# Optimization experiments

Hardware: AMD Instinct MI355X
Metric: run time of the kernel (lower is better)

Reference implementation:

```python
import jax, jax.numpy as jnp
import numpy as np

# The four fixed 2x2 patterns from the original module
PATTERNS = jnp.array([[[1, 2], [0, 0]],
                      [[0, 1], [0, 2]],
                      [[0, 0], [2, 1]],
                      [[2, 0], [1, 0]]], dtype=jnp.int32)


def setup_inputs() -> dict:
    key = jax.random.key(0)
    k1, k2 = jax.random.split(key)
    b, c, w, h = 32, 3, 1024, 1024
    x = jax.random.normal(k1, (b, c, w, h), dtype=jnp.float32)
    initmask = jax.random.randint(k2, (b, 1, w // 2, h // 2), 0, 4, dtype=jnp.int64)
    return {"x": x, "initmask": initmask}


def reference(x, initmask):
    b, c, w, h = x.shape
    # gather pattern per 2x2 block: (b, w/2, h/2, 2, 2)
    fm = PATTERNS[initmask[:, 0]]
    # interleave block dims back into full resolution: (b, 1, w, h)
    fm = fm.transpose(0, 1, 3, 2, 4).reshape(b, 1, w, h)
    mask1 = jnp.broadcast_to((fm == 1).astype(x.dtype), x.shape)
    mask2 = jnp.broadcast_to((fm == 2).astype(x.dtype), x.shape)
    return (mask1, mask2)
```

## Files before the change

kernel.cpp:

```cpp
#include <hip/hip_runtime.h>


#define N_F4_PER_OUT 25165824u

__global__ __launch_bounds__(256) void masksampling_kernel(const int* __restrict__ im,
                                                           float* __restrict__ out) {
    const unsigned t = blockIdx.x * 256u + threadIdx.x;
    const unsigned j  = t & 255u;
    const unsigned r  = (t >> 8) & 1023u;
    const unsigned bc = t >> 18;
    const unsigned b  = bc / 3u;

    const int2 m2 = ((const int2*)im)[b * 131072u + (r >> 1) * 256u + j];

    const unsigned base = (r & 1u) * 2u;
    const unsigned s0 = (unsigned)m2.x * 4u + base;
    const unsigned s1 = (unsigned)m2.y * 4u + base;

    const unsigned EQ1 = 0x4821u, EQ2 = 0x1482u;
    const float4 f1 = make_float4((float)((EQ1 >> s0) & 1u),
                                  (float)((EQ1 >> (s0 + 1u)) & 1u),
                                  (float)((EQ1 >> s1) & 1u),
                                  (float)((EQ1 >> (s1 + 1u)) & 1u));
    const float4 f2 = make_float4((float)((EQ2 >> s0) & 1u),
                                  (float)((EQ2 >> (s0 + 1u)) & 1u),
                                  (float)((EQ2 >> s1) & 1u),
                                  (float)((EQ2 >> (s1 + 1u)) & 1u));

    float4* o1 = (float4*)out;
    float4* o2 = o1 + N_F4_PER_OUT;
    o1[t] = f1;
    o2[t] = f2;
}

extern "C" void kernel_launch(void* const* d_in, const int* in_sizes, int n_in,
                              void* d_out, int out_size, void* d_ws, size_t ws_size,
                              hipStream_t stream) {
    const int* im = (const int*)d_in[1];
    float* out = (float*)d_out;
    masksampling_kernel<<<N_F4_PER_OUT / 256, 256, 0, stream>>>(im, out);
}
```

Measured before the change: 942.0 us.

## Compute each mask pair once and store both rows across all channels

Each thread now reads one int2 mask entry and writes both rows of its 2x2 block for all three channels, instead of one thread per output float4. The grid shrinks sixfold, and the redundant mask loads and per-channel recomputation are removed. The kernel stays bound by its output writes. Each thread now issues twelve strided stores, which may change coalescing and occupancy behaviour.

After: 976.9 us. 3.7% more time.

```diff
diff --git a/kernel.cpp b/kernel.cpp
--- a/kernel.cpp
+++ b/kernel.cpp
@@ -2,35 +2,49 @@
 
 
 #define N_F4_PER_OUT 25165824u
+#define N_MASK_INT2  4194304u
 
 __global__ __launch_bounds__(256) void masksampling_kernel(const int* __restrict__ im,
                                                            float* __restrict__ out) {
     const unsigned t = blockIdx.x * 256u + threadIdx.x;
     const unsigned j  = t & 255u;
-    const unsigned r  = (t >> 8) & 1023u;
-    const unsigned bc = t >> 18;
-    const unsigned b  = bc / 3u;
+    const unsigned rm = (t >> 8) & 511u;
+    const unsigned b  = t >> 17;
 
-    const int2 m2 = ((const int2*)im)[b * 131072u + (r >> 1) * 256u + j];
+    const int2 m2 = ((const int2*)im)[t];
 
-    const unsigned base = (r & 1u) * 2u;
-    const unsigned s0 = (unsigned)m2.x * 4u + base;
-    const unsigned s1 = (unsigned)m2.y * 4u + base;
+    const unsigned s0 = (unsigned)m2.x * 4u;
+    const unsigned s1 = (unsigned)m2.y * 4u;
 
     const unsigned EQ1 = 0x4821u, EQ2 = 0x1482u;
-    const float4 f1 = make_float4((float)((EQ1 >> s0) & 1u),
-                                  (float)((EQ1 >> (s0 + 1u)) & 1u),
-                                  (float)((EQ1 >> s1) & 1u),
-                                  (float)((EQ1 >> (s1 + 1u)) & 1u));
-    const float4 f2 = make_float4((float)((EQ2 >> s0) & 1u),
-                                  (float)((EQ2 >> (s0 + 1u)) & 1u),
-                                  (float)((EQ2 >> s1) & 1u),
-                                  (float)((EQ2 >> (s1 + 1u)) & 1u));
+    const float4 f1r0 = make_float4((float)((EQ1 >> s0) & 1u),
+                                    (float)((EQ1 >> (s0 + 1u)) & 1u),
+                                    (float)((EQ1 >> s1) & 1u),
+                                    (float)((EQ1 >> (s1 + 1u)) & 1u));
+    const float4 f1r1 = make_float4((float)((EQ1 >> (s0 + 2u)) & 1u),
+                                    (float)((EQ1 >> (s0 + 3u)) & 1u),
+                                    (float)((EQ1 >> (s1 + 2u)) & 1u),
+                                    (float)((EQ1 >> (s1 + 3u)) & 1u));
+    const float4 f2r0 = make_float4((float)((EQ2 >> s0) & 1u),
+                                    (float)((EQ2 >> (s0 + 1u)) & 1u),
+                                    (float)((EQ2 >> s1) & 1u),
+                                    (float)((EQ2 >> (s1 + 1u)) & 1u));
+    const float4 f2r1 = make_float4((float)((EQ2 >> (s0 + 2u)) & 1u),
+                                    (float)((EQ2 >> (s0 + 3u)) & 1u),
+                                    (float)((EQ2 >> (s1 + 2u)) & 1u),
+                                    (float)((EQ2 >> (s1 + 3u)) & 1u));
 
     float4* o1 = (float4*)out;
     float4* o2 = o1 + N_F4_PER_OUT;
-    o1[t] = f1;
-    o2[t] = f2;
+    unsigned idx = (b * 3072u + 2u * rm) * 256u + j;
+    #pragma unroll
+    for (int c = 0; c < 3; ++c) {
+        o1[idx]         = f1r0;
+        o1[idx + 256u]  = f1r1;
+        o2[idx]         = f2r0;
+        o2[idx + 256u]  = f2r1;
+        idx += 262144u;
+    }
 }
 
 extern "C" void kernel_launch(void* const* d_in, const int* in_sizes, int n_in,
@@ -38,5 +52,5 @@
                               hipStream_t stream) {
     const int* im = (const int*)d_in[1];
     float* out = (float*)d_out;
-    masksampling_kernel<<<N_F4_PER_OUT / 256, 256, 0, stream>>>(im, out);
+    masksampling_kernel<<<N_MASK_INT2 / 256, 256, 0, stream>>>(im, out);
 }
```
